# Performance work log

Hardware: AMD Instinct MI355X
Metric: run time of the kernel (lower is better)

## Reference

```python
import jax, jax.numpy as jnp
import numpy as np

# ---- static config (mirrors TALoss(num_classes=80, reg_max=16, strides=[8,16,32])) ----
B, M, NC, REG_MAX = 32, 20, 80, 16
STRIDES = (8, 16, 32)
HW = ((80, 80), (40, 40), (20, 20))          # feature map sizes for 640x640 input
NO = REG_MAX * 4 + NC                         # 144 channels per head
A = sum(h * w for h, w in HW)                 # 8400 anchors
TOPK, ALPHA, BETA = 10, 0.5, 6.0
BOX_G, CLS_G, DFL_G = 7.5, 0.5, 1.5
EPS = 1e-9


def setup_inputs() -> dict:
    key = jax.random.key(0)
    ks = jax.random.split(key, 6)
    feats = {f"feat{i}": jax.random.normal(ks[i], (B, NO, h, w), jnp.float32)
             for i, (h, w) in enumerate(HW)}
    # targets: (N,6) rows of (img_idx, class, cx, cy, w, h), normalized, 20 boxes/image, sorted by image
    img_idx = jnp.repeat(jnp.arange(B, dtype=jnp.float32), M)
    cls = jax.random.randint(ks[3], (B * M,), 0, NC).astype(jnp.float32)
    cxy = jax.random.uniform(ks[4], (B * M, 2), minval=0.2, maxval=0.8)
    wh = jax.random.uniform(ks[5], (B * M, 2), minval=0.05, maxval=0.3)
    targets = jnp.concatenate([img_idx[:, None], cls[:, None], cxy, wh], axis=1)
    return {**feats, "targets": targets}


def _make_anchors():
    pts, strs = [], []
    for (h, w), s in zip(HW, STRIDES):
        sx = jnp.arange(w, dtype=jnp.float32) + 0.5
        sy = jnp.arange(h, dtype=jnp.float32) + 0.5
        gy, gx = jnp.meshgrid(sy, sx, indexing="ij")
        pts.append(jnp.stack([gx, gy], -1).reshape(-1, 2))
        strs.append(jnp.full((h * w, 1), float(s), jnp.float32))
    return jnp.concatenate(pts), jnp.concatenate(strs)   # (A,2), (A,1)


def _ciou(b1, b2, eps=1e-7):
    # b1, b2: broadcastable xyxy boxes (..., 4) -> CIoU (...,)
    b1x1, b1y1, b1x2, b1y2 = b1[..., 0], b1[..., 1], b1[..., 2], b1[..., 3]
    b2x1, b2y1, b2x2, b2y2 = b2[..., 0], b2[..., 1], b2[..., 2], b2[..., 3]
    w1, h1 = b1x2 - b1x1, b1y2 - b1y1 + eps
    w2, h2 = b2x2 - b2x1, b2y2 - b2y1 + eps
    inter = (jnp.clip(jnp.minimum(b1x2, b2x2) - jnp.maximum(b1x1, b2x1), 0)
             * jnp.clip(jnp.minimum(b1y2, b2y2) - jnp.maximum(b1y1, b2y1), 0))
    union = w1 * h1 + w2 * h2 - inter + eps
    iou = inter / union
    cw = jnp.maximum(b1x2, b2x2) - jnp.minimum(b1x1, b2x1)
    ch = jnp.maximum(b1y2, b2y2) - jnp.minimum(b1y1, b2y1)
    c2 = cw ** 2 + ch ** 2 + eps
    rho2 = ((b2x1 + b2x2 - b1x1 - b1x2) ** 2 + (b2y1 + b2y2 - b1y1 - b1y2) ** 2) / 4.0
    v = (4.0 / np.pi ** 2) * (jnp.arctan(w2 / h2) - jnp.arctan(w1 / h1)) ** 2
    a = jax.lax.stop_gradient(v / (v - iou + (1.0 + eps)))   # torch: computed under no_grad
    return iou - (rho2 / c2 + v * a)


def _assign(pd_scores, pd_bboxes, anc, gt_labels, gt_bboxes, mask_gt):
    """TaskAlignedAssigner. pd_scores (B,A,NC) sigmoid-ed, pd_bboxes (B,A,4) image units,
    anc (A,2) image units, gt_labels (B,M), gt_bboxes (B,M,4), mask_gt (B,M) float."""
    # anchors inside each gt box -> (B,M,A)
    lt = anc[None, None, :, :] - gt_bboxes[:, :, None, :2]
    rb = gt_bboxes[:, :, None, 2:] - anc[None, None, :, :]
    mask_in = (jnp.concatenate([lt, rb], -1).min(-1) > EPS).astype(jnp.float32)
    mask = mask_in * mask_gt[..., None]                      # (B,M,A) candidate mask
    overlaps = jnp.clip(_ciou(gt_bboxes[:, :, None, :], pd_bboxes[:, None, :, :]), 0) * mask
    labels = gt_labels.astype(jnp.int32)                     # (B,M)
    # scores of each gt's class at every anchor: (B,M,A)
    bbox_scores = jnp.take_along_axis(pd_scores.transpose(0, 2, 1),
                                      jnp.broadcast_to(labels[:, :, None], (B, M, A)), axis=1) * mask
    align = (bbox_scores ** ALPHA) * (overlaps ** BETA)      # (B,M,A), already zero off-mask
    # top-k anchors per gt
    _, idxs = jax.lax.top_k(align, TOPK)                     # (B,M,K)
    idxs = jnp.where(mask_gt[..., None] > 0, idxs, 0)
    cnt = jax.nn.one_hot(idxs, A, dtype=jnp.float32).sum(-2)  # (B,M,A)
    mask_topk = jnp.where(cnt > 1, 0.0, cnt)
    mask_pos = mask_topk * mask
    # resolve anchors matched to multiple gts: keep the max-overlap gt
    fg = mask_pos.sum(1)                                     # (B,A)
    is_max = jnp.moveaxis(jax.nn.one_hot(overlaps.argmax(1), M, dtype=jnp.float32), -1, 1)  # (B,M,A)
    mask_pos = jnp.where(fg[:, None, :] > 1, is_max, mask_pos)
    fg = mask_pos.sum(1)
    tgt_idx = mask_pos.argmax(1)                             # (B,A)
    t_labels = jnp.take_along_axis(labels, tgt_idx, 1)       # (B,A)
    t_bboxes = jnp.take_along_axis(gt_bboxes, tgt_idx[..., None], 1)  # (B,A,4)
    fg_b = (fg > 0).astype(jnp.float32)
    t_scores = jax.nn.one_hot(t_labels, NC, dtype=jnp.float32) * fg_b[..., None]
    # normalize scores: align * (max overlap per gt) / (max align per gt)
    align_pos = align * mask_pos
    pos_align = align_pos.max(-1, keepdims=True)             # (B,M,1)
    pos_over = (overlaps * mask_pos).max(-1, keepdims=True)
    norm = (align_pos * pos_over / (pos_align + EPS)).max(1)  # (B,A)
    return t_bboxes, t_scores * norm[..., None], fg_b


def _forward(feat0, feat1, feat2, targets):
    feats = [feat0, feat1, feat2]
    pred = jnp.concatenate([f.reshape(B, NO, -1) for f in feats], axis=2)
    pred_distri = pred[:, :REG_MAX * 4].transpose(0, 2, 1)   # (B,A,64)
    pred_scores = pred[:, REG_MAX * 4:].transpose(0, 2, 1)   # (B,A,NC)
    anc, stride_t = _make_anchors()
    img_h, img_w = HW[0][0] * STRIDES[0], HW[0][1] * STRIDES[0]
    scale = jnp.array([img_w, img_h, img_w, img_h], jnp.float32)
    # ---- preprocess targets (N,6) -> padded (B,M,5), xywh*scale -> xyxy ----
    idx = targets[:, 0].astype(jnp.int32)
    pos = jnp.arange(targets.shape[0]) - jnp.searchsorted(idx, idx, side="left")
    out = jnp.zeros((B, M, 5), jnp.float32).at[idx, pos].set(targets[:, 1:])
    gt_labels = out[..., 0]
    xywh = out[..., 1:5] * scale
    gt_bboxes = jnp.concatenate([xywh[..., :2] - xywh[..., 2:] / 2,
                                 xywh[..., :2] + xywh[..., 2:] / 2], -1)
    mask_gt = (gt_bboxes.sum(-1) > 0).astype(jnp.float32)    # (B,M)
    # ---- DFL bbox decode (feature-map units) ----
    proj = jnp.arange(REG_MAX, dtype=jnp.float32)
    dist = jax.nn.softmax(pred_distri.reshape(B, A, 4, REG_MAX), -1) @ proj  # (B,A,4) ltrb
    pred_bboxes = jnp.concatenate([anc - dist[..., :2], anc + dist[..., 2:]], -1)
    # ---- task-aligned assignment (on detached preds, image units) ----
    pd_scores = jax.lax.stop_gradient(jax.nn.sigmoid(pred_scores))
    pd_bboxes = jax.lax.stop_gradient(pred_bboxes) * stride_t
    target_bboxes, target_scores, fg_mask = _assign(pd_scores, pd_bboxes, anc * stride_t,
                                                    gt_labels, gt_bboxes, mask_gt)
    target_bboxes = target_bboxes / stride_t
    tss = jnp.maximum(target_scores.sum(), 1.0)
    # ---- BCE-with-logits classification loss (pos_weight=1) ----
    x, t = pred_scores, target_scores
    bce = jnp.maximum(x, 0) - x * t + jnp.log1p(jnp.exp(-jnp.abs(x)))
    loss_cls = bce.sum() / tss
    # ---- CIoU box loss + DFL, weighted by per-anchor target score sum on fg ----
    weight = target_scores.sum(-1) * fg_mask                 # (B,A)
    iou = _ciou(pred_bboxes, target_bboxes)
    loss_box = ((1.0 - iou) * weight).sum() / tss
    tltrb = jnp.clip(jnp.concatenate([anc - target_bboxes[..., :2],
                                      target_bboxes[..., 2:] - anc], -1),
                     0, REG_MAX - 1 - 0.01)                  # (B,A,4)
    logp = jax.nn.log_softmax(pred_distri.reshape(B, A, 4, REG_MAX), -1)
    tl = tltrb.astype(jnp.int32)
    wl = (tl + 1).astype(jnp.float32) - tltrb
    nll_l = -jnp.take_along_axis(logp, tl[..., None], -1)[..., 0]
    nll_r = -jnp.take_along_axis(logp, (tl + 1)[..., None], -1)[..., 0]
    dfl = (nll_l * wl + nll_r * (1.0 - wl)).mean(-1)         # (B,A)
    loss_dfl = (dfl * weight).sum() / tss
    losses = jnp.stack([loss_box * BOX_G, loss_cls * CLS_G, loss_dfl * DFL_G])
    return losses.sum() * B, jax.lax.stop_gradient(losses)


def reference(feat0, feat1, feat2, targets):
    return _forward(feat0, feat1, feat2, targets)
```

## Files before the change

### kernel.cpp

```cpp
#include <hip/hip_runtime.h>
#include <math.h>

constexpr int BB  = 32;
constexpr int MM  = 20;
constexpr int NCC = 80;
constexpr int RM  = 16;
constexpr int NOC = 144;
constexpr int AT  = 8400;
constexpr int TK  = 10;
constexpr int BA  = BB * AT;
constexpr int BM  = BB * MM;
constexpr int MAXPOS = BM * TK;
constexpr int NSLOT = 1024;
constexpr float EPS_A = 1e-9f;
constexpr float VCOEF = 0.40528473456935108577551785283891f;

constexpr int NT0 = BB * 6400 / 4 / 64;
constexpr int NT1 = BB * 1600 / 4 / 64;
constexpr int NT2 = BB * 400 / 4 / 64;
constexpr int NTT = NT0 + NT1 + NT2;

struct Lvl { const float* f; int o, w, hw; float s; };

__device__ inline Lvl level_of(int a, const float* f0, const float* f1, const float* f2){
  Lvl L;
  if (a < 6400)      { L.f = f0; L.o = a;        L.w = 80; L.hw = 6400; L.s = 8.f;  }
  else if (a < 8000) { L.f = f1; L.o = a - 6400; L.w = 40; L.hw = 1600; L.s = 16.f; }
  else               { L.f = f2; L.o = a - 8000; L.w = 20; L.hw = 400;  L.s = 32.f; }
  return L;
}

__device__ inline float frcp(float x){ return __builtin_amdgcn_rcpf(x); }

__device__ inline float fast_atan(float x){
  float ax = fabsf(x);
  bool big = ax > 1.f;
  float z = big ? frcp(ax) : ax;
  float z2 = z * z;
  float p = fmaf(z2, -0.0117212f, 0.0526533f);
  p = fmaf(z2, p, -0.1164329f);
  p = fmaf(z2, p, 0.1935435f);
  p = fmaf(z2, p, -0.3326235f);
  p = fmaf(z2, p, 0.9999773f);
  float r = z * p;
  r = big ? 1.57079632679f - r : r;
  return copysignf(r, x);
}

__device__ inline float ciou_f(float b1x1,float b1y1,float b1x2,float b1y2,
                               float b2x1,float b2y1,float b2x2,float b2y2){
  const float eps = 1e-7f;
  float w1 = b1x2 - b1x1, h1 = b1y2 - b1y1 + eps;
  float w2 = b2x2 - b2x1, h2 = b2y2 - b2y1 + eps;
  float iw = fmaxf(fminf(b1x2, b2x2) - fmaxf(b1x1, b2x1), 0.f);
  float ih = fmaxf(fminf(b1y2, b2y2) - fmaxf(b1y1, b2y1), 0.f);
  float inter = iw * ih;
  float uni = w1 * h1 + w2 * h2 - inter + eps;
  float iou = inter * frcp(uni);
  float cw = fmaxf(b1x2, b2x2) - fminf(b1x1, b2x1);
  float ch = fmaxf(b1y2, b2y2) - fminf(b1y1, b2y1);
  float c2 = cw * cw + ch * ch + eps;
  float dx = b2x1 + b2x2 - b1x1 - b1x2;
  float dy = b2y1 + b2y2 - b1y1 - b1y2;
  float rho2 = (dx * dx + dy * dy) * 0.25f;
  float r1 = w1 * frcp(h1), r2 = w2 * frcp(h2);
  float dat = fast_atan((r2 - r1) * frcp(fmaf(r1, r2, 1.f)));
  float v = VCOEF * dat * dat;
  float alpha = v * frcp(v - iou + (1.0f + eps));
  return iou - (rho2 * frcp(c2) + v * alpha);
}

__device__ inline unsigned long long shfl_xor_u64(unsigned long long v, int mask){
  int lo = __shfl_xor((int)(unsigned)(v & 0xFFFFFFFFull), mask);
  int hi = __shfl_xor((int)(unsigned)(v >> 32), mask);
  return ((unsigned long long)(unsigned)hi << 32) | (unsigned)lo;
}

__device__ inline float softplus1(float x){
  return fmaxf(x, 0.f) + __logf(1.f + __expf(-fabsf(x)));
}

__device__ inline float softplus4(float4 v){
  float s = fmaxf(v.x, 0.f) + __logf(1.f + __expf(-fabsf(v.x)));
  s += fmaxf(v.y, 0.f) + __logf(1.f + __expf(-fabsf(v.y)));
  s += fmaxf(v.z, 0.f) + __logf(1.f + __expf(-fabsf(v.z)));
  s += fmaxf(v.w, 0.f) + __logf(1.f + __expf(-fabsf(v.w)));
  return s;
}

template<int HW, int W, int AOFF>
__device__ inline float fused_quad(const float* __restrict__ f, int q,
                                   float4* __restrict__ pbox,
                                   float4* __restrict__ lseg,
                                   unsigned* __restrict__ mpos){
  constexpr int HW4 = HW / 4;
  int b = q / HW4, o4 = q - b * HW4;
  int o = o4 * 4;
  const float* base = f + (size_t)b * NOC * HW + o;

  float dd[4][4], ll[4][4];
#pragma unroll
  for (int side = 0; side < 4; side++){
    float4 x[16];
#pragma unroll
    for (int j = 0; j < 16; j++)
      x[j] = *(const float4*)(base + (size_t)((side * 16 + j) * HW));
    float mx0 = x[0].x, mx1 = x[0].y, mx2 = x[0].z, mx3 = x[0].w;
#pragma unroll
    for (int j = 1; j < 16; j++){
      mx0 = fmaxf(mx0, x[j].x); mx1 = fmaxf(mx1, x[j].y);
      mx2 = fmaxf(mx2, x[j].z); mx3 = fmaxf(mx3, x[j].w);
    }
    float sm0 = 0.f, sm1 = 0.f, sm2 = 0.f, sm3 = 0.f;
    float dt0 = 0.f, dt1 = 0.f, dt2 = 0.f, dt3 = 0.f;
#pragma unroll
    for (int j = 0; j < 16; j++){
      float e0 = __expf(x[j].x - mx0), e1 = __expf(x[j].y - mx1);
      float e2 = __expf(x[j].z - mx2), e3 = __expf(x[j].w - mx3);
      sm0 += e0; sm1 += e1; sm2 += e2; sm3 += e3;
      dt0 = fmaf(e0, (float)j, dt0); dt1 = fmaf(e1, (float)j, dt1);
      dt2 = fmaf(e2, (float)j, dt2); dt3 = fmaf(e3, (float)j, dt3);
    }
    dd[side][0] = dt0 * frcp(sm0); dd[side][1] = dt1 * frcp(sm1);
    dd[side][2] = dt2 * frcp(sm2); dd[side][3] = dt3 * frcp(sm3);
    ll[side][0] = mx0 + __logf(sm0); ll[side][1] = mx1 + __logf(sm1);
    ll[side][2] = mx2 + __logf(sm2); ll[side][3] = mx3 + __logf(sm3);
  }
  int gi0 = b * AT + AOFF + o;
#pragma unroll
  for (int k = 0; k < 4; k++){
    int ok = o + k;
    int iy = ok / W;
    float ax = (float)(ok - iy * W) + 0.5f;
    float ay = (float)iy + 0.5f;
    pbox[gi0 + k] = make_float4(ax - dd[0][k], ay - dd[1][k],
                                ax + dd[2][k], ay + dd[3][k]);
    lseg[gi0 + k] = make_float4(ll[0][k], ll[1][k], ll[2][k], ll[3][k]);
  }
  *(uint4*)(&mpos[gi0]) = make_uint4(0u, 0u, 0u, 0u);

  const float* cbase = base + (size_t)(4 * RM) * HW;
  float sp = 0.f;
#pragma unroll
  for (int jj = 0; jj < NCC; jj += 8){
    float4 x[8];
#pragma unroll
    for (int j = 0; j < 8; j++)
      x[j] = *(const float4*)(cbase + (size_t)((jj + j) * HW));
#pragma unroll
    for (int j = 0; j < 8; j++)
      sp += softplus4(x[j]);
  }
  return sp;
}

__global__ __launch_bounds__(64) void k_feat4(
    const float* __restrict__ f0, const float* __restrict__ f1,
    const float* __restrict__ f2, const float* __restrict__ tgt,
    float4* __restrict__ pbox, float4* __restrict__ lse,
    unsigned* __restrict__ mpos, double* __restrict__ bce_part,
    float* __restrict__ out5, float* __restrict__ gtbox,
    int* __restrict__ gtlab, float* __restrict__ gtmask,
    int* __restrict__ pa_i, int* __restrict__ po_i,
    int* __restrict__ topk_arr, double* __restrict__ acc){
  int blk = blockIdx.x;
  int tid = threadIdx.x;
  if (blk < NTT){
    float sp;
    if (blk < NT0){
      sp = fused_quad<6400, 80, 0>(f0, blk * 64 + tid, pbox, lse, mpos);
    } else if (blk < NT0 + NT1){
      sp = fused_quad<1600, 40, 6400>(f1, (blk - NT0) * 64 + tid, pbox, lse, mpos);
    } else {
      sp = fused_quad<400, 20, 8000>(f2, (blk - NT0 - NT1) * 64 + tid, pbox, lse, mpos);
    }
    for (int off = 32; off; off >>= 1) sp += __shfl_down(sp, off);
    if (tid == 0) bce_part[blk] = (double)sp;
  } else {
    for (int i = tid; i < BM * 5; i += 64) out5[i] = 0.f;
    for (int i = tid; i < MAXPOS; i += 64) topk_arr[i] = -1;
    for (int i = tid; i < BM; i += 64){ pa_i[i] = 0; po_i[i] = 0; }
    if (tid < 8) acc[tid] = 0.0;
    __syncthreads();
    for (int t = tid; t < BM; t += 64){
      int img = (int)tgt[t * 6 + 0];
      int j = t;
      while (j > 0 && (int)tgt[(j - 1) * 6 + 0] == img) j--;
      int pos = t - j;
      if (img >= 0 && img < BB && pos < MM){
        for (int k = 0; k < 5; k++)
          out5[(img * MM + pos) * 5 + k] = tgt[t * 6 + 1 + k];
      }
    }
    __syncthreads();
    for (int t = tid; t < BM; t += 64){
      float lab = out5[t * 5 + 0];
      float cx = out5[t * 5 + 1] * 640.f;
      float cy = out5[t * 5 + 2] * 640.f;
      float w  = out5[t * 5 + 3] * 640.f;
      float h  = out5[t * 5 + 4] * 640.f;
      float x1 = cx - w * 0.5f, y1 = cy - h * 0.5f;
      float x2 = cx + w * 0.5f, y2 = cy + h * 0.5f;
      gtbox[t * 4 + 0] = x1; gtbox[t * 4 + 1] = y1;
      gtbox[t * 4 + 2] = x2; gtbox[t * 4 + 3] = y2;
      gtlab[t] = (int)lab;
      gtmask[t] = ((x1 + y1 + x2 + y2) > 0.f) ? 1.f : 0.f;
    }
  }
}

__global__ __launch_bounds__(256) void k_align(
    const float* __restrict__ f0, const float* __restrict__ f1,
    const float* __restrict__ f2, const float4* __restrict__ pbox,
    const float* __restrict__ gtbox, const int* __restrict__ gtlab,
    const float* __restrict__ gtmask,
    unsigned* __restrict__ mpos, int* __restrict__ topk_arr){
  int pair = blockIdx.x;
  int b = pair / MM, m = pair % MM;
  if (gtmask[pair] <= 0.f) return;
  int tid = threadIdx.x;
  float gx1 = gtbox[pair * 4 + 0], gy1 = gtbox[pair * 4 + 1];
  float gx2 = gtbox[pair * 4 + 2], gy2 = gtbox[pair * 4 + 3];
  int lab = gtlab[pair];
  __shared__ float s_val[NSLOT];
  __shared__ int   s_anc[NSLOT];
  __shared__ unsigned long long s_red[4];
  __shared__ int   s_win[TK];
  int base = 0;

#define PROC_LEVEL(FPTR, W, HW, AOFF, S)                                      \
  {                                                                           \
    const float s_ = (S); const float inv_ = 1.f / (S);                       \
    int x0 = max(0, (int)floorf(gx1 * inv_ - 0.5f));                          \
    int x1 = min((W) - 1, (int)ceilf(gx2 * inv_ - 0.5f));                     \
    int y0 = max(0, (int)floorf(gy1 * inv_ - 0.5f));                          \
    int y1 = min((W) - 1, (int)ceilf(gy2 * inv_ - 0.5f));                     \
    int nxx = x1 - x0 + 1, nyy = y1 - y0 + 1;                                 \
    if (nxx > 0 && nyy > 0){                                                  \
      int ntot = nxx * nyy;                                                   \
      unsigned magic = 0xFFFFFFFFu / (unsigned)nxx + 1u;                      \
      const float* clsrow = (FPTR) + (size_t)b * NOC * (HW)                   \
                            + (size_t)(4 * RM + lab) * (HW);                  \
      for (int t = tid; t < ntot; t += 256){                                  \
        int slot = base + t;                                                  \
        if (slot >= NSLOT) break;                                             \
        int iy = (int)(((unsigned long long)(unsigned)t * magic) >> 32);      \
        int ix = t - iy * nxx + x0;                                           \
        iy += y0;                                                             \
        float ax = ((float)ix + 0.5f) * s_;                                   \
        float ay = ((float)iy + 0.5f) * s_;                                   \
        float mn = fminf(fminf(ax - gx1, ay - gy1),                           \
                         fminf(gx2 - ax, gy2 - ay));                          \
        int o = iy * (W) + ix;                                                \
        int a = (AOFF) + o;                                                   \
        float aln = -1.f;                                                     \
        if (mn > EPS_A){                                                      \
          float4 pb = pbox[b * AT + a];                                       \
          float c = ciou_f(gx1, gy1, gx2, gy2,                                \
                           pb.x * s_, pb.y * s_, pb.z * s_, pb.w * s_);       \
          float ovl = fmaxf(c, 0.f);                                          \
          if (ovl > 0.f){                                                     \
            float xv = clsrow[o];                                             \
            float sc = frcp(1.f + __expf(-xv));                               \
            float o2 = ovl * ovl;                                             \
            aln = sqrtf(sc) * (o2 * o2 * o2);                                 \
          }                                                                   \
        }                                                                     \
        s_val[slot] = aln;                                                    \
        s_anc[slot] = a;                                                      \
      }                                                                       \
      base += ntot;                                                           \
    }                                                                         \
  }

  PROC_LEVEL(f0, 80, 6400, 0, 8.f)
  PROC_LEVEL(f1, 40, 1600, 6400, 16.f)
  PROC_LEVEL(f2, 20, 400, 8000, 32.f)
#undef PROC_LEVEL

  __syncthreads();
  int total = min(base, NSLOT);
  int wid = tid >> 6, lid = tid & 63;
  for (int r = 0; r < TK; r++){
    unsigned long long key = 0ULL;
    for (int i = tid; i < total; i += 256){
      float v = s_val[i];
      if (v > 0.f){
        unsigned long long k2 =
            ((unsigned long long)__float_as_uint(v) << 32) |
            (unsigned long long)(0xFFFFFFFFu - (unsigned)i);
        key = key > k2 ? key : k2;
      }
    }
    for (int xm = 1; xm < 64; xm <<= 1){
      unsigned long long o = shfl_xor_u64(key, xm);
      key = key > o ? key : o;
    }
    if (lid == 0) s_red[wid] = key;
    __syncthreads();
    if (tid == 0){
      unsigned long long k = s_red[0];
      k = k > s_red[1] ? k : s_red[1];
      k = k > s_red[2] ? k : s_red[2];
      k = k > s_red[3] ? k : s_red[3];
      if (k){
        int slot = (int)(0xFFFFFFFFu - (unsigned)(k & 0xFFFFFFFFull));
        s_win[r] = s_anc[slot];
        s_val[slot] = -1.f;
      } else s_win[r] = -1;
    }
    __syncthreads();
  }
  if (tid < TK){
    int a = s_win[tid];
    topk_arr[pair * TK + tid] = a;
    if (a >= 0) atomicOr(&mpos[(size_t)b * AT + a], 1u << m);
  }
}

__global__ __launch_bounds__(256) void k_resolve(
    const float* __restrict__ f0, const float* __restrict__ f1,
    const float* __restrict__ f2, const float4* __restrict__ pbox,
    const float* __restrict__ gtbox, const int* __restrict__ gtlab,
    const float* __restrict__ gtmask, const unsigned* __restrict__ mpos,
    const int* __restrict__ topk_arr,
    unsigned char* __restrict__ resm, float* __restrict__ resaln,
    int* __restrict__ pa_i, int* __restrict__ po_i){
  int i = blockIdx.x * 256 + threadIdx.x;
  int a = topk_arr[i];
  if (a < 0) return;
  int pair = i / TK;
  int b = pair / MM, m = pair % MM;
  unsigned bits = mpos[(size_t)b * AT + a];
  if (m != __ffs(bits) - 1) return;
  Lvl L = level_of(a, f0, f1, f2);
  float ax = ((float)(L.o % L.w) + 0.5f) * L.s;
  float ay = ((float)(L.o / L.w) + 0.5f) * L.s;
  float4 pb = pbox[b * AT + a];
  float px1 = pb.x * L.s, py1 = pb.y * L.s, px2 = pb.z * L.s, py2 = pb.w * L.s;
  int mr; float ovl;
  if (__popc(bits) > 1){
    float best = -1.f; int bm = 0;
    for (int mm = 0; mm < MM; mm++){
      float v = 0.f;
      if (gtmask[b * MM + mm] > 0.f){
        float x1 = gtbox[(b * MM + mm) * 4 + 0], y1 = gtbox[(b * MM + mm) * 4 + 1];
        float x2 = gtbox[(b * MM + mm) * 4 + 2], y2 = gtbox[(b * MM + mm) * 4 + 3];
        float mn = fminf(fminf(ax - x1, ay - y1), fminf(x2 - ax, y2 - ay));
        if (mn > EPS_A)
          v = fmaxf(ciou_f(x1, y1, x2, y2, px1, py1, px2, py2), 0.f);
      }
      if (v > best){ best = v; bm = mm; }
    }
    mr = bm; ovl = fmaxf(best, 0.f);
  } else {
    mr = m;
    float x1 = gtbox[(b * MM + mr) * 4 + 0], y1 = gtbox[(b * MM + mr) * 4 + 1];
    float x2 = gtbox[(b * MM + mr) * 4 + 2], y2 = gtbox[(b * MM + mr) * 4 + 3];
    ovl = fmaxf(ciou_f(x1, y1, x2, y2, px1, py1, px2, py2), 0.f);
  }
  int lab = gtlab[b * MM + mr];
  float xv = L.f[(size_t)b * NOC * L.hw + (size_t)(4 * RM + lab) * L.hw + L.o];
  float sc = frcp(1.f + __expf(-xv));
  float o2 = ovl * ovl;
  float aln = sqrtf(sc) * (o2 * o2 * o2);
  size_t gi = (size_t)b * AT + a;
  resm[gi] = (unsigned char)mr;
  resaln[gi] = aln;
  atomicMax(&pa_i[b * MM + mr], __float_as_int(aln));
  atomicMax(&po_i[b * MM + mr], __float_as_int(ovl));
}

__global__ __launch_bounds__(256) void k_final(
    const float* __restrict__ f0, const float* __restrict__ f1,
    const float* __restrict__ f2,
    const float4* __restrict__ pbox, const float4* __restrict__ lse,
    const float* __restrict__ gtbox, const int* __restrict__ gtlab,
    const int* __restrict__ pa_i, const int* __restrict__ po_i,
    const unsigned* __restrict__ mpos, const int* __restrict__ topk_arr,
    const unsigned char* __restrict__ resm, const float* __restrict__ resaln,
    double* __restrict__ acc){
  int i = blockIdx.x * 256 + threadIdx.x;
  float w_ = 0.f, clsp = 0.f, boxp = 0.f, dflp = 0.f;
  int a = topk_arr[i];
  if (a >= 0){
    int pair = i / TK;
    int b = pair / MM, m = pair % MM;
    unsigned bits = mpos[(size_t)b * AT + a];
    if (m == __ffs(bits) - 1){
      size_t gi = (size_t)b * AT + a;
      int mr = (int)resm[gi];
      float aln = resaln[gi];
      float pa = __int_as_float(pa_i[b * MM + mr]);
      float po = __int_as_float(po_i[b * MM + mr]);
      w_ = aln * po * frcp(pa + EPS_A);
      Lvl L = level_of(a, f0, f1, f2);
      const float* base = L.f + (size_t)b * NOC * L.hw + L.o;
      float ax = (float)(L.o % L.w) + 0.5f;
      float ay = (float)(L.o / L.w) + 0.5f;
      float inv_s = frcp(L.s);
      float tx1 = gtbox[(b * MM + mr) * 4 + 0] * inv_s, ty1 = gtbox[(b * MM + mr) * 4 + 1] * inv_s;
      float tx2 = gtbox[(b * MM + mr) * 4 + 2] * inv_s, ty2 = gtbox[(b * MM + mr) * 4 + 3] * inv_s;
      float4 pb = pbox[b * AT + a];
      float iou = ciou_f(pb.x, pb.y, pb.z, pb.w, tx1, ty1, tx2, ty2);
      boxp = (1.f - iou) * w_;
      float4 L4 = lse[b * AT + a];
      float lsv[4] = { L4.x, L4.y, L4.z, L4.w };
      float tv[4] = { ax - tx1, ay - ty1, tx2 - ax, ty2 - ay };
      float dfl = 0.f;
#pragma unroll
      for (int s4 = 0; s4 < 4; s4++){
        float t = fminf(fmaxf(tv[s4], 0.f), (float)(RM - 1) - 0.01f);
        int tl = (int)t;
        float wl = (float)(tl + 1) - t;
        float xl = base[(size_t)(s4 * RM + tl) * L.hw];
        float xr = base[(size_t)(s4 * RM + tl + 1) * L.hw];
        dfl += (lsv[s4] - xl) * wl + (lsv[s4] - xr) * (1.f - wl);
      }
      dflp = dfl * 0.25f * w_;
      int lab = gtlab[b * MM + mr];
      clsp = base[(size_t)(4 * RM + lab) * L.hw] * w_;
    }
  }
  __shared__ float red[4][4];
  float vals[4] = { w_, clsp, boxp, dflp };
  int wid = threadIdx.x >> 6, lid = threadIdx.x & 63;
#pragma unroll
  for (int j = 0; j < 4; j++){
    float v = vals[j];
    for (int off = 32; off; off >>= 1) v += __shfl_down(v, off);
    if (lid == 0) red[wid][j] = v;
  }
  __syncthreads();
  if (threadIdx.x == 0){
    float t0 = 0.f, t1 = 0.f, t2 = 0.f, t3 = 0.f;
    for (int w2 = 0; w2 < 4; w2++){
      t0 += red[w2][0]; t1 += red[w2][1]; t2 += red[w2][2]; t3 += red[w2][3];
    }
    atomicAdd(&acc[0], (double)t0);
    atomicAdd(&acc[1], (double)t1);
    atomicAdd(&acc[2], (double)t2);
    atomicAdd(&acc[3], (double)t3);
  }
}

__global__ void k_out(const double* __restrict__ acc,
                      const double* __restrict__ bce_part,
                      float* __restrict__ out){
  __shared__ double sd[256];
  double s = 0.0;
  for (int i = threadIdx.x; i < NTT; i += 256) s += bce_part[i];
  sd[threadIdx.x] = s;
  __syncthreads();
  for (int off = 128; off; off >>= 1){
    if (threadIdx.x < off) sd[threadIdx.x] += sd[threadIdx.x + off];
    __syncthreads();
  }
  if (threadIdx.x == 0){
    double bce_sum = sd[0];
    double tss = acc[0] > 1.0 ? acc[0] : 1.0;
    double loss_box = acc[2] / tss;
    double loss_cls = (bce_sum - acc[1]) / tss;
    double loss_dfl = acc[3] / tss;
    float l0 = (float)(loss_box * 7.5);
    float l1 = (float)(loss_cls * 0.5);
    float l2 = (float)(loss_dfl * 1.5);
    out[0] = (l0 + l1 + l2) * 32.f;
    out[1] = l0;
    out[2] = l1;
    out[3] = l2;
  }
}

extern "C" void kernel_launch(void* const* d_in, const int* in_sizes, int n_in,
                              void* d_out, int out_size, void* d_ws, size_t ws_size,
                              hipStream_t stream) {
  const float* f0 = (const float*)d_in[0];
  const float* f1 = (const float*)d_in[1];
  const float* f2 = (const float*)d_in[2];
  const float* tg = (const float*)d_in[3];
  float* out = (float*)d_out;

  char* w = (char*)d_ws;
  size_t off = 0;
  auto alloc = [&](size_t bytes) -> void* {
    void* p = w + off;
    off += (bytes + 255) & ~(size_t)255;
    return p;
  };
  float4*        pbox    = (float4*)       alloc((size_t)BA * 16);
  float4*        lse     = (float4*)       alloc((size_t)BA * 16);
  float*         gtbox   = (float*)        alloc((size_t)BM * 16);
  int*           gtlab   = (int*)          alloc((size_t)BM * 4);
  float*         gtmask  = (float*)        alloc((size_t)BM * 4);
  float*         out5    = (float*)        alloc((size_t)BM * 20);
  unsigned*      mpos    = (unsigned*)     alloc((size_t)BA * 4);
  int*           topk_arr= (int*)          alloc((size_t)MAXPOS * 4);
  unsigned char* resm    = (unsigned char*)alloc((size_t)BA);
  float*         resaln  = (float*)        alloc((size_t)BA * 4);
  int*           pa      = (int*)          alloc((size_t)BM * 4);
  int*           po      = (int*)          alloc((size_t)BM * 4);
  double*        acc     = (double*)       alloc(8 * 8);
  double*        bcep    = (double*)       alloc((size_t)NTT * 8);

  k_feat4<<<NTT + 1, 64, 0, stream>>>(f0, f1, f2, tg, pbox, lse, mpos, bcep,
                                      out5, gtbox, gtlab, gtmask, pa, po,
                                      topk_arr, acc);
  k_align<<<BM, 256, 0, stream>>>(f0, f1, f2, pbox, gtbox, gtlab, gtmask, mpos, topk_arr);
  k_resolve<<<MAXPOS / 256, 256, 0, stream>>>(f0, f1, f2, pbox, gtbox, gtlab, gtmask,
                                              mpos, topk_arr, resm, resaln, pa, po);
  k_final<<<MAXPOS / 256, 256, 0, stream>>>(f0, f1, f2, pbox, lse, gtbox, gtlab,
                                            pa, po, mpos, topk_arr, resm, resaln, acc);
  k_out<<<1, 256, 0, stream>>>(acc, bcep, out);
}
```

Before: 283.2 us.

## Split per-quad feature work across four threads, one per box side

The feature kernel now gives each 4-anchor quad to four threads instead of one. Each thread computes the DFL softmax for one box side and a quarter of the class softplus sum, and blocks grow from 64 to 256 threads. This quadruples thread-level parallelism and cuts per-thread register pressure and serial load chains, so the streaming read of the feature maps should hide memory latency better. In exchange, pbox and lse are written as scattered scalar floats rather than float4s, and the block-level BCE reduction needs shared memory plus a barrier.

```diff
diff --git a/kernel.cpp b/kernel.cpp
--- a/kernel.cpp
+++ b/kernel.cpp
@@ -15,9 +15,9 @@
 constexpr float EPS_A = 1e-9f;
 constexpr float VCOEF = 0.40528473456935108577551785283891f;
 
-constexpr int NT0 = BB * 6400 / 4 / 64;
-constexpr int NT1 = BB * 1600 / 4 / 64;
-constexpr int NT2 = BB * 400 / 4 / 64;
+constexpr int NT0 = BB * 6400 / 256;
+constexpr int NT1 = BB * 1600 / 256;
+constexpr int NT2 = BB * 400 / 256;
 constexpr int NTT = NT0 + NT1 + NT2;
 
 struct Lvl { const float* f; int o, w, hw; float s; };
@@ -76,10 +76,6 @@
   return ((unsigned long long)(unsigned)hi << 32) | (unsigned)lo;
 }
 
-__device__ inline float softplus1(float x){
-  return fmaxf(x, 0.f) + __logf(1.f + __expf(-fabsf(x)));
-}
-
 __device__ inline float softplus4(float4 v){
   float s = fmaxf(v.x, 0.f) + __logf(1.f + __expf(-fabsf(v.x)));
   s += fmaxf(v.y, 0.f) + __logf(1.f + __expf(-fabsf(v.y)));
@@ -89,43 +85,40 @@
 }
 
 template<int HW, int W, int AOFF>
-__device__ inline float fused_quad(const float* __restrict__ f, int q,
-                                   float4* __restrict__ pbox,
-                                   float4* __restrict__ lseg,
+__device__ inline float fused_side(const float* __restrict__ f, int t,
+                                   float* __restrict__ pbox_f,
+                                   float* __restrict__ lse_f,
                                    unsigned* __restrict__ mpos){
   constexpr int HW4 = HW / 4;
-  int b = q / HW4, o4 = q - b * HW4;
+  int lq = t >> 2, s = t & 3;
+  int b = lq / HW4, o4 = lq - b * HW4;
   int o = o4 * 4;
   const float* base = f + (size_t)b * NOC * HW + o;
 
-  float dd[4][4], ll[4][4];
-#pragma unroll
-  for (int side = 0; side < 4; side++){
-    float4 x[16];
-#pragma unroll
-    for (int j = 0; j < 16; j++)
-      x[j] = *(const float4*)(base + (size_t)((side * 16 + j) * HW));
-    float mx0 = x[0].x, mx1 = x[0].y, mx2 = x[0].z, mx3 = x[0].w;
-#pragma unroll
-    for (int j = 1; j < 16; j++){
-      mx0 = fmaxf(mx0, x[j].x); mx1 = fmaxf(mx1, x[j].y);
-      mx2 = fmaxf(mx2, x[j].z); mx3 = fmaxf(mx3, x[j].w);
-    }
-    float sm0 = 0.f, sm1 = 0.f, sm2 = 0.f, sm3 = 0.f;
-    float dt0 = 0.f, dt1 = 0.f, dt2 = 0.f, dt3 = 0.f;
-#pragma unroll
-    for (int j = 0; j < 16; j++){
-      float e0 = __expf(x[j].x - mx0), e1 = __expf(x[j].y - mx1);
-      float e2 = __expf(x[j].z - mx2), e3 = __expf(x[j].w - mx3);
-      sm0 += e0; sm1 += e1; sm2 += e2; sm3 += e3;
-      dt0 = fmaf(e0, (float)j, dt0); dt1 = fmaf(e1, (float)j, dt1);
-      dt2 = fmaf(e2, (float)j, dt2); dt3 = fmaf(e3, (float)j, dt3);
-    }
-    dd[side][0] = dt0 * frcp(sm0); dd[side][1] = dt1 * frcp(sm1);
-    dd[side][2] = dt2 * frcp(sm2); dd[side][3] = dt3 * frcp(sm3);
-    ll[side][0] = mx0 + __logf(sm0); ll[side][1] = mx1 + __logf(sm1);
-    ll[side][2] = mx2 + __logf(sm2); ll[side][3] = mx3 + __logf(sm3);
-  }
+  float4 x[16];
+#pragma unroll
+  for (int j = 0; j < 16; j++)
+    x[j] = *(const float4*)(base + (size_t)((s * 16 + j) * HW));
+  float mx0 = x[0].x, mx1 = x[0].y, mx2 = x[0].z, mx3 = x[0].w;
+#pragma unroll
+  for (int j = 1; j < 16; j++){
+    mx0 = fmaxf(mx0, x[j].x); mx1 = fmaxf(mx1, x[j].y);
+    mx2 = fmaxf(mx2, x[j].z); mx3 = fmaxf(mx3, x[j].w);
+  }
+  float sm0 = 0.f, sm1 = 0.f, sm2 = 0.f, sm3 = 0.f;
+  float dt0 = 0.f, dt1 = 0.f, dt2 = 0.f, dt3 = 0.f;
+#pragma unroll
+  for (int j = 0; j < 16; j++){
+    float e0 = __expf(x[j].x - mx0), e1 = __expf(x[j].y - mx1);
+    float e2 = __expf(x[j].z - mx2), e3 = __expf(x[j].w - mx3);
+    sm0 += e0; sm1 += e1; sm2 += e2; sm3 += e3;
+    dt0 = fmaf(e0, (float)j, dt0); dt1 = fmaf(e1, (float)j, dt1);
+    dt2 = fmaf(e2, (float)j, dt2); dt3 = fmaf(e3, (float)j, dt3);
+  }
+  float d[4]  = { dt0 * frcp(sm0), dt1 * frcp(sm1), dt2 * frcp(sm2), dt3 * frcp(sm3) };
+  float ls[4] = { mx0 + __logf(sm0), mx1 + __logf(sm1),
+                  mx2 + __logf(sm2), mx3 + __logf(sm3) };
+
   int gi0 = b * AT + AOFF + o;
 #pragma unroll
   for (int k = 0; k < 4; k++){
@@ -133,56 +126,61 @@
     int iy = ok / W;
     float ax = (float)(ok - iy * W) + 0.5f;
     float ay = (float)iy + 0.5f;
-    pbox[gi0 + k] = make_float4(ax - dd[0][k], ay - dd[1][k],
-                                ax + dd[2][k], ay + dd[3][k]);
-    lseg[gi0 + k] = make_float4(ll[0][k], ll[1][k], ll[2][k], ll[3][k]);
-  }
-  *(uint4*)(&mpos[gi0]) = make_uint4(0u, 0u, 0u, 0u);
-
-  const float* cbase = base + (size_t)(4 * RM) * HW;
+    float coord = (s == 0 || s == 2) ? ax : ay;
+    float v = (s < 2) ? (coord - d[k]) : (coord + d[k]);
+    pbox_f[(size_t)(gi0 + k) * 4 + s] = v;
+    lse_f [(size_t)(gi0 + k) * 4 + s] = ls[k];
+  }
+  if (s == 0) *(uint4*)(&mpos[gi0]) = make_uint4(0u, 0u, 0u, 0u);
+
+  const float* cbase = base + (size_t)((4 * RM) + s * 20) * HW;
   float sp = 0.f;
 #pragma unroll
-  for (int jj = 0; jj < NCC; jj += 8){
-    float4 x[8];
-#pragma unroll
-    for (int j = 0; j < 8; j++)
-      x[j] = *(const float4*)(cbase + (size_t)((jj + j) * HW));
-#pragma unroll
-    for (int j = 0; j < 8; j++)
-      sp += softplus4(x[j]);
+  for (int jj = 0; jj < 20; jj += 10){
+    float4 xx[10];
+#pragma unroll
+    for (int j = 0; j < 10; j++)
+      xx[j] = *(const float4*)(cbase + (size_t)((jj + j) * HW));
+#pragma unroll
+    for (int j = 0; j < 10; j++)
+      sp += softplus4(xx[j]);
   }
   return sp;
 }
 
-__global__ __launch_bounds__(64) void k_feat4(
+__global__ __launch_bounds__(256) void k_feat5(
     const float* __restrict__ f0, const float* __restrict__ f1,
     const float* __restrict__ f2, const float* __restrict__ tgt,
-    float4* __restrict__ pbox, float4* __restrict__ lse,
+    float* __restrict__ pbox_f, float* __restrict__ lse_f,
     unsigned* __restrict__ mpos, double* __restrict__ bce_part,
     float* __restrict__ out5, float* __restrict__ gtbox,
     int* __restrict__ gtlab, float* __restrict__ gtmask,
     int* __restrict__ pa_i, int* __restrict__ po_i,
     int* __restrict__ topk_arr, double* __restrict__ acc){
+  __shared__ float red[4];
   int blk = blockIdx.x;
   int tid = threadIdx.x;
   if (blk < NTT){
     float sp;
     if (blk < NT0){
-      sp = fused_quad<6400, 80, 0>(f0, blk * 64 + tid, pbox, lse, mpos);
+      sp = fused_side<6400, 80, 0>(f0, blk * 256 + tid, pbox_f, lse_f, mpos);
     } else if (blk < NT0 + NT1){
-      sp = fused_quad<1600, 40, 6400>(f1, (blk - NT0) * 64 + tid, pbox, lse, mpos);
+      sp = fused_side<1600, 40, 6400>(f1, (blk - NT0) * 256 + tid, pbox_f, lse_f, mpos);
     } else {
-      sp = fused_quad<400, 20, 8000>(f2, (blk - NT0 - NT1) * 64 + tid, pbox, lse, mpos);
+      sp = fused_side<400, 20, 8000>(f2, (blk - NT0 - NT1) * 256 + tid, pbox_f, lse_f, mpos);
     }
     for (int off = 32; off; off >>= 1) sp += __shfl_down(sp, off);
-    if (tid == 0) bce_part[blk] = (double)sp;
+    int wid = tid >> 6, lid = tid & 63;
+    if (lid == 0) red[wid] = sp;
+    __syncthreads();
+    if (tid == 0) bce_part[blk] = (double)(red[0] + red[1] + red[2] + red[3]);
   } else {
-    for (int i = tid; i < BM * 5; i += 64) out5[i] = 0.f;
-    for (int i = tid; i < MAXPOS; i += 64) topk_arr[i] = -1;
-    for (int i = tid; i < BM; i += 64){ pa_i[i] = 0; po_i[i] = 0; }
+    for (int i = tid; i < BM * 5; i += 256) out5[i] = 0.f;
+    for (int i = tid; i < MAXPOS; i += 256) topk_arr[i] = -1;
+    for (int i = tid; i < BM; i += 256){ pa_i[i] = 0; po_i[i] = 0; }
     if (tid < 8) acc[tid] = 0.0;
     __syncthreads();
-    for (int t = tid; t < BM; t += 64){
+    for (int t = tid; t < BM; t += 256){
       int img = (int)tgt[t * 6 + 0];
       int j = t;
       while (j > 0 && (int)tgt[(j - 1) * 6 + 0] == img) j--;
@@ -193,7 +191,7 @@
       }
     }
     __syncthreads();
-    for (int t = tid; t < BM; t += 64){
+    for (int t = tid; t < BM; t += 256){
       float lab = out5[t * 5 + 0];
       float cx = out5[t * 5 + 1] * 640.f;
       float cy = out5[t * 5 + 2] * 640.f;
@@ -503,9 +501,9 @@
   double*        acc     = (double*)       alloc(8 * 8);
   double*        bcep    = (double*)       alloc((size_t)NTT * 8);
 
-  k_feat4<<<NTT + 1, 64, 0, stream>>>(f0, f1, f2, tg, pbox, lse, mpos, bcep,
-                                      out5, gtbox, gtlab, gtmask, pa, po,
-                                      topk_arr, acc);
+  k_feat5<<<NTT + 1, 256, 0, stream>>>(f0, f1, f2, tg, (float*)pbox, (float*)lse,
+                                       mpos, bcep, out5, gtbox, gtlab, gtmask,
+                                       pa, po, topk_arr, acc);
   k_align<<<BM, 256, 0, stream>>>(f0, f1, f2, pbox, gtbox, gtlab, gtmask, mpos, topk_arr);
   k_resolve<<<MAXPOS / 256, 256, 0, stream>>>(f0, f1, f2, pbox, gtbox, gtlab, gtmask,
                                               mpos, topk_arr, resm, resaln, pa, po);
```

Result: faster. 249.0 us (-12.1%).
